# Kernel tuning notes

Hardware: AMD Instinct MI355X
Metric: run time of the kernel (lower is better)

Reference implementation:

```python
import jax, jax.numpy as jnp
import numpy as np

IMG_FEAT = 2048
HIDDEN = 512


def setup_inputs() -> dict:
    key = jax.random.key(0)
    ks = jax.random.split(key, 9)
    B, R = 512, 10
    img = jax.random.normal(ks[0], (B * R, IMG_FEAT), dtype=jnp.float32)
    ques = jax.random.normal(ks[1], (B * R, HIDDEN), dtype=jnp.float32)
    hist = jax.random.normal(ks[2], (B * R, R, HIDDEN), dtype=jnp.float32)
    fusion = IMG_FEAT + HIDDEN
    # kaiming-uniform-ish init scales
    W_fuse = jax.random.uniform(ks[3], (HIDDEN, fusion), dtype=jnp.float32,
                                minval=-1.0, maxval=1.0) * np.sqrt(6.0 / fusion)
    b_fuse = jnp.zeros((HIDDEN,), dtype=jnp.float32)
    w_att = jax.random.uniform(ks[4], (HIDDEN,), dtype=jnp.float32,
                               minval=-1.0, maxval=1.0) * np.sqrt(6.0 / HIDDEN)
    b_att = jnp.zeros((), dtype=jnp.float32)
    W_hist = jax.random.uniform(ks[5], (HIDDEN, HIDDEN), dtype=jnp.float32,
                                minval=-1.0, maxval=1.0) * np.sqrt(6.0 / HIDDEN)
    b_hist = jnp.zeros((HIDDEN,), dtype=jnp.float32)
    return {
        "img": img, "ques": ques, "hist": hist,
        "W_fuse": W_fuse, "b_fuse": b_fuse,
        "w_att": w_att, "b_att": b_att,
        "W_hist": W_hist, "b_hist": b_hist,
        "batch_size": B, "num_rounds": R,
    }


def reference(img, ques, hist, W_fuse, b_fuse, w_att, b_att, W_hist, b_hist,
              batch_size, num_rounds):
    # Dropout is identity (eval mode).
    BR = batch_size * num_rounds
    # fused embedding: tanh(Linear(cat(img, ques)))  -> [B*R, D]
    fused_vec = jnp.concatenate([img, ques], axis=1)
    fused = jnp.tanh(fused_vec @ W_fuse.T + b_fuse)
    D = fused.shape[-1]
    hist_r = hist.reshape(BR, num_rounds, D)  # [B*R, R, D]
    # scores: (hist * broadcast(fused)) @ w_att + b_att  -> [B*R, R]
    # equivalent to the repeat + elementwise-mul + linear-to-scalar in torch
    scores = jnp.einsum('brd,bd,d->br', hist_r, fused, w_att) + b_att
    attn = jax.nn.softmax(scores, axis=1)  # softmax over num_rounds
    hist_embed = jnp.einsum('br,brd->bd', attn, hist_r)  # weighted sum
    hist_embed = jnp.tanh(hist_embed @ W_hist.T + b_hist)
    out = fused + hist_embed
    return out.reshape(batch_size, num_rounds, D)
```

## Files before the change

kernel.cpp:

```cpp
#include <hip/hip_runtime.h>
#include <hip/hip_bf16.h>

#define HIDDEN 512
#define IMGF   2048
#define RNDS   10

typedef float  f32x4  __attribute__((ext_vector_type(4)));
typedef __bf16 bf16x8 __attribute__((ext_vector_type(8)));
typedef unsigned short u16x8 __attribute__((ext_vector_type(8)));

__device__ __forceinline__ unsigned short f2bf(float x) {
    union { float f; unsigned u; } v; v.f = x;
    unsigned r = v.u + 0x7FFFu + ((v.u >> 16) & 1u);
    return (unsigned short)(r >> 16);
}
__device__ __forceinline__ float bf2f(unsigned short h) {
    union { unsigned u; float f; } v; v.u = ((unsigned)h) << 16;
    return v.f;
}

__device__ __forceinline__ void cp16_async(const void* g, void* l) {
    __builtin_amdgcn_global_load_lds(
        (const __attribute__((address_space(1))) unsigned int*)g,
        (__attribute__((address_space(3))) unsigned int*)l,
        16, 0, 0);
}

__global__ __launch_bounds__(256)
void cvt_bf16(const float* __restrict__ p0, long n0,
              const float* __restrict__ p1, long n1,
              const float* __restrict__ p2, long n2,
              const float* __restrict__ p3, long n3,
              unsigned short* __restrict__ q0, unsigned short* __restrict__ q1,
              unsigned short* __restrict__ q2, unsigned short* __restrict__ q3)
{
    long i = ((long)blockIdx.x * 256 + threadIdx.x) * 4;
    const float* s; unsigned short* d; long j;
    if      (i < n0)            { s = p0; d = q0; j = i; }
    else if (i < n0 + n1)       { s = p1; d = q1; j = i - n0; }
    else if (i < n0 + n1 + n2)  { s = p2; d = q2; j = i - n0 - n1; }
    else                        { s = p3; d = q3; j = i - n0 - n1 - n2; }
    float4 v = *(const float4*)(s + j);
    ushort4 o;
    o.x = f2bf(v.x); o.y = f2bf(v.y); o.z = f2bf(v.z); o.w = f2bf(v.w);
    *(ushort4*)(d + j) = o;
}

template<bool RESID>
__global__ __launch_bounds__(256, 4)
void gemm_bt_tanh(const unsigned short* __restrict__ A0, int lda0,
                  const unsigned short* __restrict__ A1, int lda1, int kSplit,
                  const unsigned short* __restrict__ W,
                  const float* __restrict__ bias,
                  const unsigned short* __restrict__ residb,
                  float* __restrict__ outf, unsigned short* __restrict__ outb,
                  int K)
{
    __shared__ unsigned short lA[2][32 * 64];
    __shared__ unsigned short lB[2][64 * 64];

    const int bm = blockIdx.x * 32;
    const int bn = blockIdx.y * 64;
    const int t    = threadIdx.x;
    const int lane = t & 63;
    const int wave = t >> 6;
    const int wm = (wave >> 1) * 16;
    const int wn = (wave & 1) * 32;
    const int lr = lane & 15;
    const int lq = lane >> 4;

    const unsigned short* Wb0 = W + (size_t)bn * K;

    auto stage_tiles = [&](int kt, int buf) {
        int k0 = kt << 6;
        const unsigned short* Ab; int lda;
        if (k0 < kSplit) { Ab = A0 + (size_t)bm * lda0 + k0;            lda = lda0; }
        else             { Ab = A1 + (size_t)bm * lda1 + (k0 - kSplit); lda = lda1; }
        {
            int r = t >> 3, s = (t & 7) ^ (r & 7);
            cp16_async(Ab + (size_t)r * lda + s * 8, &lA[buf][t * 8]);
        }
        #pragma unroll
        for (int h = 0; h < 2; ++h) {
            int ci = h * 256 + t;
            int r = ci >> 3, s = (ci & 7) ^ (r & 7);
            cp16_async(Wb0 + k0 + (size_t)r * K + s * 8, &lB[buf][ci * 8]);
        }
    };

    f32x4 acc[2] = {};
    const int NT = K >> 6;

    stage_tiles(0, 0);
    for (int kt = 0; kt < NT; ++kt) {
        __syncthreads();
        if (kt + 1 < NT) stage_tiles(kt + 1, (kt + 1) & 1);
        const unsigned short* a = &lA[kt & 1][0];
        const unsigned short* b = &lB[kt & 1][0];
        #pragma unroll
        for (int kh = 0; kh < 2; ++kh) {
            const int c = kh * 4 + lq;
            const int ra = wm + lr;
            bf16x8 af = __builtin_bit_cast(bf16x8,
                *(const u16x8*)&a[ra * 64 + ((c ^ (ra & 7)) * 8)]);
            #pragma unroll
            for (int ni = 0; ni < 2; ++ni) {
                const int rb = wn + ni * 16 + lr;
                bf16x8 bf = __builtin_bit_cast(bf16x8,
                    *(const u16x8*)&b[rb * 64 + ((c ^ (rb & 7)) * 8)]);
                acc[ni] = __builtin_amdgcn_mfma_f32_16x16x32_bf16(
                    af, bf, acc[ni], 0, 0, 0);
            }
        }
    }

    #pragma unroll
    for (int ni = 0; ni < 2; ++ni) {
        const int col = bn + wn + ni * 16 + lr;
        const float bc = bias[col];
        const int rbase = bm + wm + lq * 4;
        #pragma unroll
        for (int j = 0; j < 4; ++j) {
            const size_t idx = (size_t)(rbase + j) * HIDDEN + col;
            float v = tanhf(acc[ni][j] + bc);
            if (RESID) outf[idx] = v + bf2f(residb[idx]);
            else       outb[idx] = f2bf(v);
        }
    }
}

__global__ __launch_bounds__(256)
void attn_embed(const float* __restrict__ hist,
                const unsigned short* __restrict__ fusedb,
                const float* __restrict__ w_att,
                const float* __restrict__ b_att,
                unsigned short* __restrict__ hembed)
{
    const int lane = threadIdx.x & 63;
    const int wave = threadIdx.x >> 6;
    const int b = blockIdx.x * 4 + wave;
    const int d = lane * 8;

    float g[8];
    {
        u16x8 f = *(const u16x8*)(fusedb + (size_t)b * HIDDEN + d);
        const float4 w0 = *(const float4*)(w_att + d);
        const float4 w1 = *(const float4*)(w_att + d + 4);
        g[0]=bf2f(f[0])*w0.x; g[1]=bf2f(f[1])*w0.y; g[2]=bf2f(f[2])*w0.z; g[3]=bf2f(f[3])*w0.w;
        g[4]=bf2f(f[4])*w1.x; g[5]=bf2f(f[5])*w1.y; g[6]=bf2f(f[6])*w1.z; g[7]=bf2f(f[7])*w1.w;
    }
    const float* hb = hist + (size_t)b * RNDS * HIDDEN + d;

    float h[RNDS][8], p[RNDS];
    #pragma unroll
    for (int r = 0; r < RNDS; ++r) {
        const float4 a0 = *(const float4*)(hb + r * HIDDEN);
        const float4 a1 = *(const float4*)(hb + r * HIDDEN + 4);
        h[r][0]=a0.x; h[r][1]=a0.y; h[r][2]=a0.z; h[r][3]=a0.w;
        h[r][4]=a1.x; h[r][5]=a1.y; h[r][6]=a1.z; h[r][7]=a1.w;
        float s = 0.f;
        #pragma unroll
        for (int i = 0; i < 8; ++i) s += h[r][i] * g[i];
        p[r] = s;
    }
    #pragma unroll
    for (int r = 0; r < RNDS; ++r)
        #pragma unroll
        for (int m = 1; m < 64; m <<= 1)
            p[r] += __shfl_xor(p[r], m, 64);

    const float ba = b_att[0];
    float mx = -1e30f;
    #pragma unroll
    for (int r = 0; r < RNDS; ++r) mx = fmaxf(mx, p[r] + ba);
    float sum = 0.f, a[RNDS];
    #pragma unroll
    for (int r = 0; r < RNDS; ++r) { a[r] = __expf(p[r] + ba - mx); sum += a[r]; }
    const float inv = 1.0f / sum;

    float e[8] = {};
    #pragma unroll
    for (int r = 0; r < RNDS; ++r)
        #pragma unroll
        for (int i = 0; i < 8; ++i) e[i] += a[r] * h[r][i];

    ushort4 o0, o1;
    o0.x=f2bf(e[0]*inv); o0.y=f2bf(e[1]*inv); o0.z=f2bf(e[2]*inv); o0.w=f2bf(e[3]*inv);
    o1.x=f2bf(e[4]*inv); o1.y=f2bf(e[5]*inv); o1.z=f2bf(e[6]*inv); o1.w=f2bf(e[7]*inv);
    unsigned short* q = hembed + (size_t)b * HIDDEN + d;
    *(ushort4*)q = o0;
    *(ushort4*)(q + 4) = o1;
}

extern "C" void kernel_launch(void* const* d_in, const int* in_sizes, int n_in,
                              void* d_out, int out_size, void* d_ws, size_t ws_size,
                              hipStream_t stream)
{
    const float* img    = (const float*)d_in[0];
    const float* ques   = (const float*)d_in[1];
    const float* hist   = (const float*)d_in[2];
    const float* W_fuse = (const float*)d_in[3];
    const float* b_fuse = (const float*)d_in[4];
    const float* w_att  = (const float*)d_in[5];
    const float* b_att  = (const float*)d_in[6];
    const float* W_hist = (const float*)d_in[7];
    const float* b_hist = (const float*)d_in[8];

    const long n_img  = in_sizes[0];
    const long n_ques = in_sizes[1];
    const long n_Wf   = in_sizes[3];
    const long n_Wh   = in_sizes[7];
    const int  BR     = (int)(n_ques / HIDDEN);

    unsigned short* imgb   = (unsigned short*)d_ws;
    unsigned short* quesb  = imgb   + n_img;
    unsigned short* Wfb    = quesb  + n_ques;
    unsigned short* Whb    = Wfb    + n_Wf;
    unsigned short* fusedb = Whb    + n_Wh;
    unsigned short* hembb  = fusedb + (size_t)BR * HIDDEN;

    const long total4 = (n_img + n_ques + n_Wf + n_Wh) / 4;
    cvt_bf16<<<dim3((unsigned)((total4 + 255) / 256)), dim3(256), 0, stream>>>(
        img, n_img, ques, n_ques, W_fuse, n_Wf, W_hist, n_Wh,
        imgb, quesb, Wfb, Whb);

    dim3 blk(256);
    dim3 g1(BR / 32, HIDDEN / 64);

    gemm_bt_tanh<false><<<g1, blk, 0, stream>>>(
        imgb, IMGF, quesb, HIDDEN, IMGF,
        Wfb, b_fuse, nullptr, nullptr, fusedb, IMGF + HIDDEN);

    attn_embed<<<dim3(BR / 4), blk, 0, stream>>>(hist, fusedb, w_att, b_att, hembb);

    gemm_bt_tanh<true><<<g1, blk, 0, stream>>>(
        hembb, HIDDEN, nullptr, 0, HIDDEN,
        Whb, b_hist, fusedb, (float*)d_out, nullptr, HIDDEN);
}
```

Measured before the change: 256.4 us.

## Fuse all stages into one persistent kernel with grid barriers

Replaces the four launches (bf16 conversion, fuse GEMM, attention, hist GEMM) with a single persistent kernel of 640 blocks separated by atomic spin grid barriers. The GEMM tile grows to 64x64 with 2x2 MFMA accumulators per wave, and tiles are mapped per XCD for locality. The aim is to remove launch gaps and tail effects, in exchange for barrier spin cost and a reliance on all 640 blocks being co-resident (occupancy 3 per CU), otherwise the kernel deadlocks.

```diff
diff --git a/kernel.cpp b/kernel.cpp
--- a/kernel.cpp
+++ b/kernel.cpp
@@ -4,6 +4,7 @@
 #define HIDDEN 512
 #define IMGF   2048
 #define RNDS   10
+#define NBLK   640
 
 typedef float  f32x4  __attribute__((ext_vector_type(4)));
 typedef __bf16 bf16x8 __attribute__((ext_vector_type(8)));
@@ -26,170 +27,199 @@
         16, 0, 0);
 }
 
-__global__ __launch_bounds__(256)
-void cvt_bf16(const float* __restrict__ p0, long n0,
-              const float* __restrict__ p1, long n1,
-              const float* __restrict__ p2, long n2,
-              const float* __restrict__ p3, long n3,
-              unsigned short* __restrict__ q0, unsigned short* __restrict__ q1,
-              unsigned short* __restrict__ q2, unsigned short* __restrict__ q3)
+#define GRID_BARRIER(CNT)                                              \
+    __syncthreads();                                                   \
+    if (t == 0) {                                                      \
+        __threadfence();                                               \
+        atomicAdd((CNT), 1u);                                          \
+        while (atomicAdd((CNT), 0u) < NBLK) { }                        \
+        __threadfence();                                               \
+    }                                                                  \
+    __syncthreads();
+
+#define STAGE_TILES(KT, BUF) {                                          \
+    int k0_ = (KT) << 6;                                                \
+    const unsigned short* Ab_; int lda_;                                \
+    if (k0_ < g_ks) { Ab_ = g_A0 + (size_t)bm * g_lda0 + k0_;            lda_ = g_lda0; } \
+    else            { Ab_ = g_A1 + (size_t)bm * g_lda1 + (k0_ - g_ks);   lda_ = g_lda1; } \
+    for (int h_ = 0; h_ < 2; ++h_) {                                    \
+        int ci_ = h_ * 256 + t;                                         \
+        int r_ = ci_ >> 3, s_ = (ci_ & 7) ^ (r_ & 7);                   \
+        cp16_async(Ab_ + (size_t)r_ * lda_ + s_ * 8, &lA[BUF][ci_ * 8]); \
+        cp16_async(g_Wb + k0_ + (size_t)r_ * g_K + s_ * 8, &lB[BUF][ci_ * 8]); \
+    } }
+
+#define GEMM_KLOOP(NT)                                                  \
+    STAGE_TILES(0, 0);                                                  \
+    for (int kt = 0; kt < (NT); ++kt) {                                 \
+        __syncthreads();                                                \
+        if (kt + 1 < (NT)) STAGE_TILES(kt + 1, (kt + 1) & 1);           \
+        const unsigned short* a_ = &lA[kt & 1][0];                      \
+        const unsigned short* b_ = &lB[kt & 1][0];                      \
+        for (int kh = 0; kh < 2; ++kh) {                                \
+            const int c_ = kh * 4 + lq;                                 \
+            const int ra0 = wm + lr,      ra1 = wm + 16 + lr;           \
+            const int rb0 = wn + lr,      rb1 = wn + 16 + lr;           \
+            bf16x8 af0 = __builtin_bit_cast(bf16x8, *(const u16x8*)&a_[ra0 * 64 + ((c_ ^ (ra0 & 7)) * 8)]); \
+            bf16x8 af1 = __builtin_bit_cast(bf16x8, *(const u16x8*)&a_[ra1 * 64 + ((c_ ^ (ra1 & 7)) * 8)]); \
+            bf16x8 bf0 = __builtin_bit_cast(bf16x8, *(const u16x8*)&b_[rb0 * 64 + ((c_ ^ (rb0 & 7)) * 8)]); \
+            bf16x8 bf1 = __builtin_bit_cast(bf16x8, *(const u16x8*)&b_[rb1 * 64 + ((c_ ^ (rb1 & 7)) * 8)]); \
+            acc00 = __builtin_amdgcn_mfma_f32_16x16x32_bf16(af0, bf0, acc00, 0, 0, 0); \
+            acc01 = __builtin_amdgcn_mfma_f32_16x16x32_bf16(af0, bf1, acc01, 0, 0, 0); \
+            acc10 = __builtin_amdgcn_mfma_f32_16x16x32_bf16(af1, bf0, acc10, 0, 0, 0); \
+            acc11 = __builtin_amdgcn_mfma_f32_16x16x32_bf16(af1, bf1, acc11, 0, 0, 0); \
+        }                                                               \
+    }                                                                   \
+    __syncthreads();
+
+#define EPI_BF16(ACC, MI, NI, BIAS, DST) {                              \
+    const int col_ = bn + wn + (NI) * 16 + lr;                          \
+    const float bc_ = (BIAS)[col_];                                     \
+    const int rb_ = bm + wm + (MI) * 16 + lq * 4;                       \
+    for (int j_ = 0; j_ < 4; ++j_) {                                    \
+        const size_t idx_ = (size_t)(rb_ + j_) * HIDDEN + col_;         \
+        (DST)[idx_] = f2bf(tanhf(ACC[j_] + bc_));                       \
+    } }
+
+#define EPI_RESID(ACC, MI, NI, BIAS, RESB, DST) {                       \
+    const int col_ = bn + wn + (NI) * 16 + lr;                          \
+    const float bc_ = (BIAS)[col_];                                     \
+    const int rb_ = bm + wm + (MI) * 16 + lq * 4;                       \
+    for (int j_ = 0; j_ < 4; ++j_) {                                    \
+        const size_t idx_ = (size_t)(rb_ + j_) * HIDDEN + col_;         \
+        (DST)[idx_] = tanhf(ACC[j_] + bc_) + bf2f((RESB)[idx_]);        \
+    } }
+
+__global__ __launch_bounds__(256, 3)
+void mega(const float* __restrict__ img,   const float* __restrict__ ques,
+          const float* __restrict__ hist,
+          const float* __restrict__ b_fuse, const float* __restrict__ w_att,
+          const float* __restrict__ b_att,  const float* __restrict__ b_hist,
+          const float* __restrict__ W_fuse, const float* __restrict__ W_hist,
+          unsigned short* __restrict__ imgb,   unsigned short* __restrict__ quesb,
+          unsigned short* __restrict__ Wfb,    unsigned short* __restrict__ Whb,
+          unsigned short* __restrict__ fusedb, unsigned short* __restrict__ hembb,
+          float* __restrict__ out, unsigned* __restrict__ bar,
+          long n_img, long n_ques, long n_Wf, long n_Wh, int BR)
 {
-    long i = ((long)blockIdx.x * 256 + threadIdx.x) * 4;
-    const float* s; unsigned short* d; long j;
-    if      (i < n0)            { s = p0; d = q0; j = i; }
-    else if (i < n0 + n1)       { s = p1; d = q1; j = i - n0; }
-    else if (i < n0 + n1 + n2)  { s = p2; d = q2; j = i - n0 - n1; }
-    else                        { s = p3; d = q3; j = i - n0 - n1 - n2; }
-    float4 v = *(const float4*)(s + j);
-    ushort4 o;
-    o.x = f2bf(v.x); o.y = f2bf(v.y); o.z = f2bf(v.z); o.w = f2bf(v.w);
-    *(ushort4*)(d + j) = o;
-}
-
-template<bool RESID>
-__global__ __launch_bounds__(256, 4)
-void gemm_bt_tanh(const unsigned short* __restrict__ A0, int lda0,
-                  const unsigned short* __restrict__ A1, int lda1, int kSplit,
-                  const unsigned short* __restrict__ W,
-                  const float* __restrict__ bias,
-                  const unsigned short* __restrict__ residb,
-                  float* __restrict__ outf, unsigned short* __restrict__ outb,
-                  int K)
-{
-    __shared__ unsigned short lA[2][32 * 64];
+    __shared__ unsigned short lA[2][64 * 64];
     __shared__ unsigned short lB[2][64 * 64];
 
-    const int bm = blockIdx.x * 32;
-    const int bn = blockIdx.y * 64;
     const int t    = threadIdx.x;
     const int lane = t & 63;
     const int wave = t >> 6;
-    const int wm = (wave >> 1) * 16;
+    const int bx   = blockIdx.x;
+
+    {
+        const long total  = n_img + n_ques + n_Wf + n_Wh;
+        const long stride = (long)NBLK * 256 * 4;
+        for (long i = ((long)bx * 256 + t) * 4; i < total; i += stride) {
+            const float* sp; unsigned short* dp; long j;
+            if      (i < n_img)                  { sp = img;    dp = imgb;  j = i; }
+            else if (i < n_img + n_ques)         { sp = ques;   dp = quesb; j = i - n_img; }
+            else if (i < n_img + n_ques + n_Wf)  { sp = W_fuse; dp = Wfb;   j = i - n_img - n_ques; }
+            else                                 { sp = W_hist; dp = Whb;   j = i - n_img - n_ques - n_Wf; }
+            float4 v = *(const float4*)(sp + j);
+            ushort4 o;
+            o.x = f2bf(v.x); o.y = f2bf(v.y); o.z = f2bf(v.z); o.w = f2bf(v.w);
+            *(ushort4*)(dp + j) = o;
+        }
+    }
+    GRID_BARRIER(bar + 0)
+
+    const int xcd = bx & 7, bj = bx >> 3;
+    const int bm  = (xcd * 10 + (bj % 10)) * 64;
+    const int bn  = (bj / 10) * 64;
+
+    const int wm = (wave >> 1) * 32;
     const int wn = (wave & 1) * 32;
     const int lr = lane & 15;
     const int lq = lane >> 4;
 
-    const unsigned short* Wb0 = W + (size_t)bn * K;
-
-    auto stage_tiles = [&](int kt, int buf) {
-        int k0 = kt << 6;
-        const unsigned short* Ab; int lda;
-        if (k0 < kSplit) { Ab = A0 + (size_t)bm * lda0 + k0;            lda = lda0; }
-        else             { Ab = A1 + (size_t)bm * lda1 + (k0 - kSplit); lda = lda1; }
-        {
-            int r = t >> 3, s = (t & 7) ^ (r & 7);
-            cp16_async(Ab + (size_t)r * lda + s * 8, &lA[buf][t * 8]);
-        }
-        #pragma unroll
-        for (int h = 0; h < 2; ++h) {
-            int ci = h * 256 + t;
-            int r = ci >> 3, s = (ci & 7) ^ (r & 7);
-            cp16_async(Wb0 + k0 + (size_t)r * K + s * 8, &lB[buf][ci * 8]);
-        }
-    };
-
-    f32x4 acc[2] = {};
-    const int NT = K >> 6;
-
-    stage_tiles(0, 0);
-    for (int kt = 0; kt < NT; ++kt) {
-        __syncthreads();
-        if (kt + 1 < NT) stage_tiles(kt + 1, (kt + 1) & 1);
-        const unsigned short* a = &lA[kt & 1][0];
-        const unsigned short* b = &lB[kt & 1][0];
-        #pragma unroll
-        for (int kh = 0; kh < 2; ++kh) {
-            const int c = kh * 4 + lq;
-            const int ra = wm + lr;
-            bf16x8 af = __builtin_bit_cast(bf16x8,
-                *(const u16x8*)&a[ra * 64 + ((c ^ (ra & 7)) * 8)]);
-            #pragma unroll
-            for (int ni = 0; ni < 2; ++ni) {
-                const int rb = wn + ni * 16 + lr;
-                bf16x8 bf = __builtin_bit_cast(bf16x8,
-                    *(const u16x8*)&b[rb * 64 + ((c ^ (rb & 7)) * 8)]);
-                acc[ni] = __builtin_amdgcn_mfma_f32_16x16x32_bf16(
-                    af, bf, acc[ni], 0, 0, 0);
+    {
+        const unsigned short* g_A0 = imgb;  const int g_lda0 = IMGF;
+        const unsigned short* g_A1 = quesb; const int g_lda1 = HIDDEN;
+        const int g_ks = IMGF;
+        const int g_K  = IMGF + HIDDEN;
+        const unsigned short* g_Wb = Wfb + (size_t)bn * g_K;
+        f32x4 acc00 = {}, acc01 = {}, acc10 = {}, acc11 = {};
+        GEMM_KLOOP(40)
+        EPI_BF16(acc00, 0, 0, b_fuse, fusedb)
+        EPI_BF16(acc01, 0, 1, b_fuse, fusedb)
+        EPI_BF16(acc10, 1, 0, b_fuse, fusedb)
+        EPI_BF16(acc11, 1, 1, b_fuse, fusedb)
+    }
+    GRID_BARRIER(bar + 16)
+
+    {
+        const float ba = b_att[0];
+        const int gw = bx * 4 + wave;
+        for (int rr = 0; rr < 2; ++rr) {
+            const int b = gw * 2 + rr;
+            if (b < BR) {
+                const int d = lane * 8;
+                float g[8];
+                {
+                    u16x8 f = *(const u16x8*)(fusedb + (size_t)b * HIDDEN + d);
+                    const float4 w0 = *(const float4*)(w_att + d);
+                    const float4 w1 = *(const float4*)(w_att + d + 4);
+                    g[0]=bf2f(f[0])*w0.x; g[1]=bf2f(f[1])*w0.y;
+                    g[2]=bf2f(f[2])*w0.z; g[3]=bf2f(f[3])*w0.w;
+                    g[4]=bf2f(f[4])*w1.x; g[5]=bf2f(f[5])*w1.y;
+                    g[6]=bf2f(f[6])*w1.z; g[7]=bf2f(f[7])*w1.w;
+                }
+                const float* hb = hist + (size_t)b * RNDS * HIDDEN + d;
+
+                float h[RNDS][8], p[RNDS];
+                for (int r = 0; r < RNDS; ++r) {
+                    const float4 a0 = *(const float4*)(hb + r * HIDDEN);
+                    const float4 a1 = *(const float4*)(hb + r * HIDDEN + 4);
+                    h[r][0]=a0.x; h[r][1]=a0.y; h[r][2]=a0.z; h[r][3]=a0.w;
+                    h[r][4]=a1.x; h[r][5]=a1.y; h[r][6]=a1.z; h[r][7]=a1.w;
+                    float s = 0.f;
+                    for (int i = 0; i < 8; ++i) s += h[r][i] * g[i];
+                    p[r] = s;
+                }
+                for (int r = 0; r < RNDS; ++r)
+                    for (int m = 1; m < 64; m <<= 1)
+                        p[r] += __shfl_xor(p[r], m, 64);
+
+                float mx = -1e30f;
+                for (int r = 0; r < RNDS; ++r) mx = fmaxf(mx, p[r] + ba);
+                float sum = 0.f, a[RNDS];
+                for (int r = 0; r < RNDS; ++r) { a[r] = __expf(p[r] + ba - mx); sum += a[r]; }
+                const float inv = 1.0f / sum;
+
+                float e[8] = {};
+                for (int r = 0; r < RNDS; ++r)
+                    for (int i = 0; i < 8; ++i) e[i] += a[r] * h[r][i];
+
+                ushort4 o0, o1;
+                o0.x=f2bf(e[0]*inv); o0.y=f2bf(e[1]*inv);
+                o0.z=f2bf(e[2]*inv); o0.w=f2bf(e[3]*inv);
+                o1.x=f2bf(e[4]*inv); o1.y=f2bf(e[5]*inv);
+                o1.z=f2bf(e[6]*inv); o1.w=f2bf(e[7]*inv);
+                unsigned short* q = hembb + (size_t)b * HIDDEN + d;
+                *(ushort4*)q = o0;
+                *(ushort4*)(q + 4) = o1;
             }
         }
     }
-
-    #pragma unroll
-    for (int ni = 0; ni < 2; ++ni) {
-        const int col = bn + wn + ni * 16 + lr;
-        const float bc = bias[col];
-        const int rbase = bm + wm + lq * 4;
-        #pragma unroll
-        for (int j = 0; j < 4; ++j) {
-            const size_t idx = (size_t)(rbase + j) * HIDDEN + col;
-            float v = tanhf(acc[ni][j] + bc);
-            if (RESID) outf[idx] = v + bf2f(residb[idx]);
-            else       outb[idx] = f2bf(v);
-        }
-    }
-}
-
-__global__ __launch_bounds__(256)
-void attn_embed(const float* __restrict__ hist,
-                const unsigned short* __restrict__ fusedb,
-                const float* __restrict__ w_att,
-                const float* __restrict__ b_att,
-                unsigned short* __restrict__ hembed)
-{
-    const int lane = threadIdx.x & 63;
-    const int wave = threadIdx.x >> 6;
-    const int b = blockIdx.x * 4 + wave;
-    const int d = lane * 8;
-
-    float g[8];
-    {
-        u16x8 f = *(const u16x8*)(fusedb + (size_t)b * HIDDEN + d);
-        const float4 w0 = *(const float4*)(w_att + d);
-        const float4 w1 = *(const float4*)(w_att + d + 4);
-        g[0]=bf2f(f[0])*w0.x; g[1]=bf2f(f[1])*w0.y; g[2]=bf2f(f[2])*w0.z; g[3]=bf2f(f[3])*w0.w;
-        g[4]=bf2f(f[4])*w1.x; g[5]=bf2f(f[5])*w1.y; g[6]=bf2f(f[6])*w1.z; g[7]=bf2f(f[7])*w1.w;
-    }
-    const float* hb = hist + (size_t)b * RNDS * HIDDEN + d;
-
-    float h[RNDS][8], p[RNDS];
-    #pragma unroll
-    for (int r = 0; r < RNDS; ++r) {
-        const float4 a0 = *(const float4*)(hb + r * HIDDEN);
-        const float4 a1 = *(const float4*)(hb + r * HIDDEN + 4);
-        h[r][0]=a0.x; h[r][1]=a0.y; h[r][2]=a0.z; h[r][3]=a0.w;
-        h[r][4]=a1.x; h[r][5]=a1.y; h[r][6]=a1.z; h[r][7]=a1.w;
-        float s = 0.f;
-        #pragma unroll
-        for (int i = 0; i < 8; ++i) s += h[r][i] * g[i];
-        p[r] = s;
-    }
-    #pragma unroll
-    for (int r = 0; r < RNDS; ++r)
-        #pragma unroll
-        for (int m = 1; m < 64; m <<= 1)
-            p[r] += __shfl_xor(p[r], m, 64);
-
-    const float ba = b_att[0];
-    float mx = -1e30f;
-    #pragma unroll
-    for (int r = 0; r < RNDS; ++r) mx = fmaxf(mx, p[r] + ba);
-    float sum = 0.f, a[RNDS];
-    #pragma unroll
-    for (int r = 0; r < RNDS; ++r) { a[r] = __expf(p[r] + ba - mx); sum += a[r]; }
-    const float inv = 1.0f / sum;
-
-    float e[8] = {};
-    #pragma unroll
-    for (int r = 0; r < RNDS; ++r)
-        #pragma unroll
-        for (int i = 0; i < 8; ++i) e[i] += a[r] * h[r][i];
-
-    ushort4 o0, o1;
-    o0.x=f2bf(e[0]*inv); o0.y=f2bf(e[1]*inv); o0.z=f2bf(e[2]*inv); o0.w=f2bf(e[3]*inv);
-    o1.x=f2bf(e[4]*inv); o1.y=f2bf(e[5]*inv); o1.z=f2bf(e[6]*inv); o1.w=f2bf(e[7]*inv);
-    unsigned short* q = hembed + (size_t)b * HIDDEN + d;
-    *(ushort4*)q = o0;
-    *(ushort4*)(q + 4) = o1;
+    GRID_BARRIER(bar + 32)
+
+    {
+        const unsigned short* g_A0 = hembb; const int g_lda0 = HIDDEN;
+        const unsigned short* g_A1 = hembb; const int g_lda1 = HIDDEN;
+        const int g_ks = HIDDEN;
+        const int g_K  = HIDDEN;
+        const unsigned short* g_Wb = Whb + (size_t)bn * g_K;
+        f32x4 acc00 = {}, acc01 = {}, acc10 = {}, acc11 = {};
+        GEMM_KLOOP(8)
+        EPI_RESID(acc00, 0, 0, b_hist, fusedb, out)
+        EPI_RESID(acc01, 0, 1, b_hist, fusedb, out)
+        EPI_RESID(acc10, 1, 0, b_hist, fusedb, out)
+        EPI_RESID(acc11, 1, 1, b_hist, fusedb, out)
+    }
 }
 
 extern "C" void kernel_launch(void* const* d_in, const int* in_sizes, int n_in,
@@ -206,11 +236,11 @@
     const float* W_hist = (const float*)d_in[7];
     const float* b_hist = (const float*)d_in[8];
 
-    const long n_img  = in_sizes[0];
-    const long n_ques = in_sizes[1];
-    const long n_Wf   = in_sizes[3];
-    const long n_Wh   = in_sizes[7];
-    const int  BR     = (int)(n_ques / HIDDEN);
+    long n_img  = in_sizes[0];
+    long n_ques = in_sizes[1];
+    long n_Wf   = in_sizes[3];
+    long n_Wh   = in_sizes[7];
+    int  BR     = (int)(n_ques / HIDDEN);
 
     unsigned short* imgb   = (unsigned short*)d_ws;
     unsigned short* quesb  = imgb   + n_img;
@@ -218,22 +248,15 @@
     unsigned short* Whb    = Wfb    + n_Wf;
     unsigned short* fusedb = Whb    + n_Wh;
     unsigned short* hembb  = fusedb + (size_t)BR * HIDDEN;
-
-    const long total4 = (n_img + n_ques + n_Wf + n_Wh) / 4;
-    cvt_bf16<<<dim3((unsigned)((total4 + 255) / 256)), dim3(256), 0, stream>>>(
-        img, n_img, ques, n_ques, W_fuse, n_Wf, W_hist, n_Wh,
-        imgb, quesb, Wfb, Whb);
-
-    dim3 blk(256);
-    dim3 g1(BR / 32, HIDDEN / 64);
-
-    gemm_bt_tanh<false><<<g1, blk, 0, stream>>>(
-        imgb, IMGF, quesb, HIDDEN, IMGF,
-        Wfb, b_fuse, nullptr, nullptr, fusedb, IMGF + HIDDEN);
-
-    attn_embed<<<dim3(BR / 4), blk, 0, stream>>>(hist, fusedb, w_att, b_att, hembb);
-
-    gemm_bt_tanh<true><<<g1, blk, 0, stream>>>(
-        hembb, HIDDEN, nullptr, 0, HIDDEN,
-        Whb, b_hist, fusedb, (float*)d_out, nullptr, HIDDEN);
-}
+    size_t bar_off = (size_t)((char*)(hembb + (size_t)BR * HIDDEN) - (char*)d_ws);
+    bar_off = (bar_off + 255) & ~(size_t)255;
+    unsigned* bar = (unsigned*)((char*)d_ws + bar_off);
+    float* outp = (float*)d_out;
+
+    hipMemsetAsync(bar, 0, 48 * sizeof(unsigned), stream);
+
+    mega<<<dim3(NBLK), dim3(256), 0, stream>>>(
+        img, ques, hist, b_fuse, w_att, b_att, b_hist, W_fuse, W_hist,
+        imgb, quesb, Wfb, Whb, fusedb, hembb, outp, bar,
+        n_img, n_ques, n_Wf, n_Wh, BR);
+}
```

Result: slower. 465.7 us (+81.6%).
